# Performance work log

Hardware: AMD Instinct MI355X
Metric: run time of the kernel (lower is better)

Reference implementation:

```python
import jax, jax.numpy as jnp
import numpy as np

NEG_INF = float("-inf")
WINDOW = 5  # window_size in LocalAttention; half = WINDOW // 2 = 2


def setup_inputs() -> dict:
    key = jax.random.key(0)
    kq, kk, kv = jax.random.split(key, 3)
    B, L, H, E = 4, 2048, 8, 64
    queries = jax.random.normal(kq, (B, L, H, E), dtype=jnp.float32)
    keys = jax.random.normal(kk, (B, L, H, E), dtype=jnp.float32)
    values = jax.random.normal(kv, (B, L, H, E), dtype=jnp.float32)
    return {"queries": queries, "keys": keys, "values": values}


def reference(queries, keys, values):
    # queries/keys/values: [B, L, H, E]; dropout is identity (eval mode).
    B, L, H, E = queries.shape
    scale = 1.0 / jnp.sqrt(jnp.asarray(E, dtype=queries.dtype))
    # Shared scores for both branches: [B, H, L, S]
    scores = jnp.einsum("blhe,bshe->bhls", queries, keys)

    # Global (unmasked) branch
    A_global = jax.nn.softmax(scale * scores, axis=-1)

    # Local branch: torch mask allows j in [max(i-2,0), min(i+2,L)) => i-2 <= j <= i+1
    half = WINDOW // 2
    i = jnp.arange(L)[:, None]
    j = jnp.arange(L)[None, :]
    allowed = (j - i >= -half) & (j - i < half)  # [L, L], asymmetric window
    local_scores = jnp.where(allowed, scores, NEG_INF)
    A_local = jax.nn.softmax(scale * local_scores, axis=-1)

    # Sum of the two attention outputs == (A_global + A_local) @ V
    out = jnp.einsum("bhls,bshd->blhd", A_global + A_local, values)
    return out
```

## Files before the change

### kernel.cpp

```cpp
#include <hip/hip_runtime.h>
#include <hip/hip_bf16.h>
#include <stdint.h>


#define LQ 2048
#define HQ 8
#define EQ 64
#define BQ 4
#define BM 64
#define BN 64
#define RS (HQ * EQ)
#define SCALE_LOG2E 0.18033688011112042f
#define NTILE (LQ / BN)
#define TILE_U32 2048
#define IMG_U32 (BQ * HQ * NTILE * TILE_U32)

typedef __attribute__((ext_vector_type(8))) short bf16x8;
typedef __attribute__((ext_vector_type(4))) float f32x4;
typedef __attribute__((ext_vector_type(4))) unsigned int u32x4;

static __device__ __forceinline__ unsigned int f2bf(float f) {
    union { float f; unsigned int u; } c; c.f = f;
    return (c.u + 0x8000u) >> 16;
}
static __device__ __forceinline__ unsigned int pk2(float lo, float hi) {
    union { float f; unsigned int u; } a, b; a.f = lo; b.f = hi;
    return ((a.u + 0x8000u) >> 16) | ((b.u + 0x8000u) & 0xffff0000u);
}
static __device__ __forceinline__ void gload16(const uint32_t* g, void* l) {
    __builtin_amdgcn_global_load_lds(
        (const __attribute__((address_space(1))) unsigned int*)g,
        (__attribute__((address_space(3))) unsigned int*)l, 16, 0, 0);
}

__global__ __launch_bounds__(256) void prepack_kernel(
    const float* __restrict__ K, const float* __restrict__ V,
    uint32_t* __restrict__ Kimg, uint32_t* __restrict__ Vimg)
{
    const int tid = threadIdx.x;
    const int jc  = blockIdx.x;
    const int bh  = blockIdx.y;
    const int b   = bh >> 3;
    const int h   = bh & 7;
    const int j0  = jc * BN;
    const float* Kbh = K + (size_t)b * LQ * RS + h * EQ;
    const float* Vbh = V + (size_t)b * LQ * RS + h * EQ;
    uint32_t* Kt = Kimg + (size_t)(bh * NTILE + jc) * TILE_U32;
    uint32_t* Vt = Vimg + (size_t)(bh * NTILE + jc) * TILE_U32;

    #pragma unroll
    for (int it = 0; it < 2; ++it) {
        int t2 = tid + it * 256;
        int jr = t2 >> 3, eo = t2 & 7;
        const float* src = Kbh + (size_t)(j0 + jr) * RS + eo * 8;
        float4 a  = *(const float4*)src;
        float4 bv = *(const float4*)(src + 4);
        u32x4 p;
        p.x = pk2(a.x, a.y);   p.y = pk2(a.z, a.w);
        p.z = pk2(bv.x, bv.y); p.w = pk2(bv.z, bv.w);
        *(u32x4*)&Kt[jr * 32 + ((eo ^ (jr & 7)) << 2)] = p;
    }
    #pragma unroll
    for (int it = 0; it < 2; ++it) {
        int t2 = tid + it * 256;
        int e = t2 & 63, jo = t2 >> 6;
        const float* src = Vbh + (size_t)(j0 + jo * 8) * RS + e;
        float v0 = src[0 * RS], v1 = src[1 * RS], v2 = src[2 * RS], v3 = src[3 * RS];
        float v4 = src[4 * RS], v5 = src[5 * RS], v6 = src[6 * RS], v7 = src[7 * RS];
        u32x4 p;
        p.x = pk2(v0, v1); p.y = pk2(v2, v3);
        p.z = pk2(v4, v5); p.w = pk2(v6, v7);
        *(u32x4*)&Vt[e * 32 + ((jo ^ (e & 7)) << 2)] = p;
    }
}

__global__ __launch_bounds__(256) void hybrid_attn_fast(
    const float* __restrict__ Q, const float* __restrict__ K,
    const float* __restrict__ V, const uint32_t* __restrict__ Kimg,
    const uint32_t* __restrict__ Vimg, float* __restrict__ O)
{
    __shared__ unsigned short Ks[64 * 64];
    __shared__ unsigned short Vt[64 * 64];
    __shared__ unsigned short Ps[4][16 * 64];
    __shared__ float sloc[BM][4];

    const int tid  = threadIdx.x;
    const int wave = tid >> 6;
    const int lane = tid & 63;
    const int c    = lane & 15;
    const int g    = lane >> 4;
    const int qt   = blockIdx.x;
    const int bh   = blockIdx.y;
    const int b    = bh >> 3;
    const int h    = bh & 7;
    const int i0   = qt * BM;

    const float* Qbh = Q + (size_t)b * LQ * RS + h * EQ;
    const float* Kbh = K + (size_t)b * LQ * RS + h * EQ;
    const float* Vbh = V + (size_t)b * LQ * RS + h * EQ;
    float*       Obh = O + (size_t)b * LQ * RS + h * EQ;

    bf16x8 qf[2];
    {
        const int iA = i0 + wave * 16 + c;
        const float* qrow = Qbh + (size_t)iA * RS + g * 8;
        #pragma unroll
        for (int f = 0; f < 2; ++f) {
            float4 a  = *(const float4*)(qrow + f * 32);
            float4 bv = *(const float4*)(qrow + f * 32 + 4);
            union { bf16x8 v; unsigned int u[4]; } fr;
            fr.u[0] = pk2(a.x  * SCALE_LOG2E, a.y  * SCALE_LOG2E);
            fr.u[1] = pk2(a.z  * SCALE_LOG2E, a.w  * SCALE_LOG2E);
            fr.u[2] = pk2(bv.x * SCALE_LOG2E, bv.y * SCALE_LOG2E);
            fr.u[3] = pk2(bv.z * SCALE_LOG2E, bv.w * SCALE_LOG2E);
            qf[f] = fr.v;
        }
    }

    int kfo[4][2], vfo[4][2], pfo[2], pso[4][4];
    #pragma unroll
    for (int n = 0; n < 4; ++n)
        #pragma unroll
        for (int f = 0; f < 2; ++f)
            kfo[n][f] = (n * 16 + c) * 64 + ((((f << 2) | g) ^ (c & 7)) << 3);
    #pragma unroll
    for (int eg = 0; eg < 4; ++eg)
        #pragma unroll
        for (int kh = 0; kh < 2; ++kh)
            vfo[eg][kh] = (eg * 16 + c) * 64 + ((((kh << 2) | g) ^ (c & 7)) << 3);
    #pragma unroll
    for (int kh = 0; kh < 2; ++kh)
        pfo[kh] = c * 64 + ((((kh << 2) | g) ^ (c & 7)) << 3);
    #pragma unroll
    for (int r = 0; r < 4; ++r) {
        const int row = g * 4 + r;
        #pragma unroll
        for (int n = 0; n < 4; ++n) {
            const int col = n * 16 + c;
            pso[r][n] = row * 64 + ((((col >> 3) ^ (row & 7)) << 3) | (col & 7));
        }
    }

    f32x4 oacc[4];
    #pragma unroll
    for (int eg = 0; eg < 4; ++eg) oacc[eg] = (f32x4){0.f, 0.f, 0.f, 0.f};
    float l_r[4] = {0.f, 0.f, 0.f, 0.f};

    const uint32_t* kgb = Kimg + (size_t)bh * (NTILE * TILE_U32) + (wave * 2) * 256 + lane * 4;
    const uint32_t* vgb = Vimg + (size_t)bh * (NTILE * TILE_U32) + (wave * 2) * 256 + lane * 4;
    unsigned short* ksl0 = &Ks[(wave * 2) * 512];
    unsigned short* ksl1 = &Ks[(wave * 2 + 1) * 512];
    unsigned short* vtl0 = &Vt[(wave * 2) * 512];
    unsigned short* vtl1 = &Vt[(wave * 2 + 1) * 512];

    for (int jc = 0; jc < NTILE; ++jc) {
        __syncthreads();
        const uint32_t* kg = kgb + jc * TILE_U32;
        const uint32_t* vg = vgb + jc * TILE_U32;
        gload16(kg,       ksl0);
        gload16(kg + 256, ksl1);
        gload16(vg,       vtl0);
        gload16(vg + 256, vtl1);
        __syncthreads();

        f32x4 sf[4];
        #pragma unroll
        for (int n = 0; n < 4; ++n) {
            bf16x8 k0 = *(const bf16x8*)&Ks[kfo[n][0]];
            bf16x8 k1 = *(const bf16x8*)&Ks[kfo[n][1]];
            f32x4 acc = (f32x4){0.f, 0.f, 0.f, 0.f};
            acc = __builtin_amdgcn_mfma_f32_16x16x32_bf16(qf[0], k0, acc, 0, 0, 0);
            acc = __builtin_amdgcn_mfma_f32_16x16x32_bf16(qf[1], k1, acc, 0, 0, 0);
            sf[n] = acc;
        }

        #pragma unroll
        for (int r = 0; r < 4; ++r) {
            float p0 = exp2f(sf[0][r]);
            float p1 = exp2f(sf[1][r]);
            float p2 = exp2f(sf[2][r]);
            float p3 = exp2f(sf[3][r]);
            l_r[r] += (p0 + p1) + (p2 + p3);
            Ps[wave][pso[r][0]] = (unsigned short)f2bf(p0);
            Ps[wave][pso[r][1]] = (unsigned short)f2bf(p1);
            Ps[wave][pso[r][2]] = (unsigned short)f2bf(p2);
            Ps[wave][pso[r][3]] = (unsigned short)f2bf(p3);
        }
        asm volatile("s_waitcnt lgkmcnt(0)" ::: "memory");

        bf16x8 pf0 = *(const bf16x8*)&Ps[wave][pfo[0]];
        bf16x8 pf1 = *(const bf16x8*)&Ps[wave][pfo[1]];
        #pragma unroll
        for (int eg = 0; eg < 4; ++eg) {
            bf16x8 v0 = *(const bf16x8*)&Vt[vfo[eg][0]];
            bf16x8 v1 = *(const bf16x8*)&Vt[vfo[eg][1]];
            oacc[eg] = __builtin_amdgcn_mfma_f32_16x16x32_bf16(pf0, v0, oacc[eg], 0, 0, 0);
            oacc[eg] = __builtin_amdgcn_mfma_f32_16x16x32_bf16(pf1, v1, oacc[eg], 0, 0, 0);
        }
    }

    #pragma unroll
    for (int r = 0; r < 4; ++r) {
        float l = l_r[r];
        l += __shfl_xor(l, 1);
        l += __shfl_xor(l, 2);
        l += __shfl_xor(l, 4);
        l += __shfl_xor(l, 8);
        l_r[r] = 1.0f / l;
    }

    {
        const int br = tid >> 2;
        const int jj = tid & 3;
        const int i  = i0 + br;
        const int j  = i - 2 + jj;
        float s = -INFINITY;
        if (j >= 0 && j < LQ) {
            const float* qrow = Qbh + (size_t)i * RS;
            const float* krow = Kbh + (size_t)j * RS;
            float acc = 0.f;
            #pragma unroll
            for (int e = 0; e < 64; e += 4) {
                float4 qa = *(const float4*)(qrow + e);
                float4 ka = *(const float4*)(krow + e);
                acc = fmaf(qa.x, ka.x, acc); acc = fmaf(qa.y, ka.y, acc);
                acc = fmaf(qa.z, ka.z, acc); acc = fmaf(qa.w, ka.w, acc);
            }
            s = 0.125f * acc;
        }
        sloc[br][jj] = s;
    }
    __syncthreads();

    #pragma unroll
    for (int r = 0; r < 4; ++r) {
        const int row = wave * 16 + g * 4 + r;
        const int i   = i0 + row;
        float s0 = sloc[row][0], s1 = sloc[row][1], s2 = sloc[row][2], s3 = sloc[row][3];
        float mx = fmaxf(fmaxf(s0, s1), fmaxf(s2, s3));
        float w0 = expf(s0 - mx), w1 = expf(s1 - mx);
        float w2 = expf(s2 - mx), w3 = expf(s3 - mx);
        float inv = 1.0f / (w0 + w1 + w2 + w3);
        w0 *= inv; w1 *= inv; w2 *= inv; w3 *= inv;
        const float li = l_r[r];
        float* orow = Obh + (size_t)i * RS;
        #pragma unroll
        for (int eg = 0; eg < 4; ++eg) {
            const int e = eg * 16 + c;
            float val = oacc[eg][r] * li;
            if (w0 > 0.f) val += w0 * Vbh[(size_t)(i - 2) * RS + e];
            if (w1 > 0.f) val += w1 * Vbh[(size_t)(i - 1) * RS + e];
            if (w2 > 0.f) val += w2 * Vbh[(size_t)(i    ) * RS + e];
            if (w3 > 0.f) val += w3 * Vbh[(size_t)(i + 1) * RS + e];
            orow[e] = val;
        }
    }
}

__global__ __launch_bounds__(256) void hybrid_attn_fb(
    const float* __restrict__ Q, const float* __restrict__ K,
    const float* __restrict__ V, float* __restrict__ O)
{
    __shared__ unsigned short Ks[64 * 64];
    __shared__ unsigned short Vt[64 * 64];
    __shared__ unsigned short Ps[4][16 * 64];
    __shared__ float sloc[BM][4];

    const int tid  = threadIdx.x;
    const int wave = tid >> 6;
    const int lane = tid & 63;
    const int c    = lane & 15;
    const int g    = lane >> 4;
    const int qt   = blockIdx.x;
    const int bh   = blockIdx.y;
    const int b    = bh >> 3;
    const int h    = bh & 7;
    const int i0   = qt * BM;

    const float* Qbh = Q + (size_t)b * LQ * RS + h * EQ;
    const float* Kbh = K + (size_t)b * LQ * RS + h * EQ;
    const float* Vbh = V + (size_t)b * LQ * RS + h * EQ;
    float*       Obh = O + (size_t)b * LQ * RS + h * EQ;

    bf16x8 qf[2];
    {
        const int iA = i0 + wave * 16 + c;
        const float* qrow = Qbh + (size_t)iA * RS + g * 8;
        #pragma unroll
        for (int f = 0; f < 2; ++f) {
            float4 a  = *(const float4*)(qrow + f * 32);
            float4 bv = *(const float4*)(qrow + f * 32 + 4);
            union { bf16x8 v; unsigned int u[4]; } fr;
            fr.u[0] = pk2(a.x  * SCALE_LOG2E, a.y  * SCALE_LOG2E);
            fr.u[1] = pk2(a.z  * SCALE_LOG2E, a.w  * SCALE_LOG2E);
            fr.u[2] = pk2(bv.x * SCALE_LOG2E, bv.y * SCALE_LOG2E);
            fr.u[3] = pk2(bv.z * SCALE_LOG2E, bv.w * SCALE_LOG2E);
            qf[f] = fr.v;
        }
    }

    int kfo[4][2], vfo[4][2], pfo[2], pso[4][4];
    #pragma unroll
    for (int n = 0; n < 4; ++n)
        #pragma unroll
        for (int f = 0; f < 2; ++f)
            kfo[n][f] = (n * 16 + c) * 64 + ((((f << 2) | g) ^ (c & 7)) << 3);
    #pragma unroll
    for (int eg = 0; eg < 4; ++eg)
        #pragma unroll
        for (int kh = 0; kh < 2; ++kh)
            vfo[eg][kh] = (eg * 16 + c) * 64 + ((((kh << 2) | g) ^ (c & 7)) << 3);
    #pragma unroll
    for (int kh = 0; kh < 2; ++kh)
        pfo[kh] = c * 64 + ((((kh << 2) | g) ^ (c & 7)) << 3);
    #pragma unroll
    for (int r = 0; r < 4; ++r) {
        const int row = g * 4 + r;
        #pragma unroll
        for (int n = 0; n < 4; ++n) {
            const int col = n * 16 + c;
            pso[r][n] = row * 64 + ((((col >> 3) ^ (row & 7)) << 3) | (col & 7));
        }
    }

    f32x4 oacc[4];
    #pragma unroll
    for (int eg = 0; eg < 4; ++eg) oacc[eg] = (f32x4){0.f, 0.f, 0.f, 0.f};
    float l_r[4] = {0.f, 0.f, 0.f, 0.f};

    for (int j0 = 0; j0 < LQ; j0 += BN) {
        __syncthreads();
        #pragma unroll
        for (int it = 0; it < 2; ++it) {
            int t2 = tid + it * 256;
            int jr = t2 >> 3, eo = t2 & 7;
            const float* src = Kbh + (size_t)(j0 + jr) * RS + eo * 8;
            float4 a  = *(const float4*)src;
            float4 bv = *(const float4*)(src + 4);
            u32x4 p;
            p.x = pk2(a.x, a.y);   p.y = pk2(a.z, a.w);
            p.z = pk2(bv.x, bv.y); p.w = pk2(bv.z, bv.w);
            *(u32x4*)&Ks[jr * 64 + ((eo ^ (jr & 7)) << 3)] = p;
        }
        #pragma unroll
        for (int it = 0; it < 2; ++it) {
            int t2 = tid + it * 256;
            int e = t2 & 63, jo = t2 >> 6;
            const float* src = Vbh + (size_t)(j0 + jo * 8) * RS + e;
            float v0 = src[0 * RS], v1 = src[1 * RS], v2 = src[2 * RS], v3 = src[3 * RS];
            float v4 = src[4 * RS], v5 = src[5 * RS], v6 = src[6 * RS], v7 = src[7 * RS];
            u32x4 p;
            p.x = pk2(v0, v1); p.y = pk2(v2, v3);
            p.z = pk2(v4, v5); p.w = pk2(v6, v7);
            *(u32x4*)&Vt[e * 64 + ((jo ^ (e & 7)) << 3)] = p;
        }
        __syncthreads();

        f32x4 sf[4];
        #pragma unroll
        for (int n = 0; n < 4; ++n) {
            bf16x8 k0 = *(const bf16x8*)&Ks[kfo[n][0]];
            bf16x8 k1 = *(const bf16x8*)&Ks[kfo[n][1]];
            f32x4 acc = (f32x4){0.f, 0.f, 0.f, 0.f};
            acc = __builtin_amdgcn_mfma_f32_16x16x32_bf16(qf[0], k0, acc, 0, 0, 0);
            acc = __builtin_amdgcn_mfma_f32_16x16x32_bf16(qf[1], k1, acc, 0, 0, 0);
            sf[n] = acc;
        }
        #pragma unroll
        for (int r = 0; r < 4; ++r) {
            float p0 = exp2f(sf[0][r]);
            float p1 = exp2f(sf[1][r]);
            float p2 = exp2f(sf[2][r]);
            float p3 = exp2f(sf[3][r]);
            l_r[r] += (p0 + p1) + (p2 + p3);
            Ps[wave][pso[r][0]] = (unsigned short)f2bf(p0);
            Ps[wave][pso[r][1]] = (unsigned short)f2bf(p1);
            Ps[wave][pso[r][2]] = (unsigned short)f2bf(p2);
            Ps[wave][pso[r][3]] = (unsigned short)f2bf(p3);
        }
        asm volatile("s_waitcnt lgkmcnt(0)" ::: "memory");

        bf16x8 pf0 = *(const bf16x8*)&Ps[wave][pfo[0]];
        bf16x8 pf1 = *(const bf16x8*)&Ps[wave][pfo[1]];
        #pragma unroll
        for (int eg = 0; eg < 4; ++eg) {
            bf16x8 v0 = *(const bf16x8*)&Vt[vfo[eg][0]];
            bf16x8 v1 = *(const bf16x8*)&Vt[vfo[eg][1]];
            oacc[eg] = __builtin_amdgcn_mfma_f32_16x16x32_bf16(pf0, v0, oacc[eg], 0, 0, 0);
            oacc[eg] = __builtin_amdgcn_mfma_f32_16x16x32_bf16(pf1, v1, oacc[eg], 0, 0, 0);
        }
    }

    #pragma unroll
    for (int r = 0; r < 4; ++r) {
        float l = l_r[r];
        l += __shfl_xor(l, 1);
        l += __shfl_xor(l, 2);
        l += __shfl_xor(l, 4);
        l += __shfl_xor(l, 8);
        l_r[r] = 1.0f / l;
    }

    {
        const int br = tid >> 2;
        const int jj = tid & 3;
        const int i  = i0 + br;
        const int j  = i - 2 + jj;
        float s = -INFINITY;
        if (j >= 0 && j < LQ) {
            const float* qrow = Qbh + (size_t)i * RS;
            const float* krow = Kbh + (size_t)j * RS;
            float acc = 0.f;
            #pragma unroll
            for (int e = 0; e < 64; e += 4) {
                float4 qa = *(const float4*)(qrow + e);
                float4 ka = *(const float4*)(krow + e);
                acc = fmaf(qa.x, ka.x, acc); acc = fmaf(qa.y, ka.y, acc);
                acc = fmaf(qa.z, ka.z, acc); acc = fmaf(qa.w, ka.w, acc);
            }
            s = 0.125f * acc;
        }
        sloc[br][jj] = s;
    }
    __syncthreads();

    #pragma unroll
    for (int r = 0; r < 4; ++r) {
        const int row = wave * 16 + g * 4 + r;
        const int i   = i0 + row;
        float s0 = sloc[row][0], s1 = sloc[row][1], s2 = sloc[row][2], s3 = sloc[row][3];
        float mx = fmaxf(fmaxf(s0, s1), fmaxf(s2, s3));
        float w0 = expf(s0 - mx), w1 = expf(s1 - mx);
        float w2 = expf(s2 - mx), w3 = expf(s3 - mx);
        float inv = 1.0f / (w0 + w1 + w2 + w3);
        w0 *= inv; w1 *= inv; w2 *= inv; w3 *= inv;
        const float li = l_r[r];
        float* orow = Obh + (size_t)i * RS;
        #pragma unroll
        for (int eg = 0; eg < 4; ++eg) {
            const int e = eg * 16 + c;
            float val = oacc[eg][r] * li;
            if (w0 > 0.f) val += w0 * Vbh[(size_t)(i - 2) * RS + e];
            if (w1 > 0.f) val += w1 * Vbh[(size_t)(i - 1) * RS + e];
            if (w2 > 0.f) val += w2 * Vbh[(size_t)(i    ) * RS + e];
            if (w3 > 0.f) val += w3 * Vbh[(size_t)(i + 1) * RS + e];
            orow[e] = val;
        }
    }
}

extern "C" void kernel_launch(void* const* d_in, const int* in_sizes, int n_in,
                              void* d_out, int out_size, void* d_ws, size_t ws_size,
                              hipStream_t stream) {
    (void)in_sizes; (void)n_in; (void)out_size;
    const float* Q = (const float*)d_in[0];
    const float* K = (const float*)d_in[1];
    const float* V = (const float*)d_in[2];
    float* O = (float*)d_out;
    dim3 grid(LQ / BM, BQ * HQ);
    const size_t need = (size_t)2 * IMG_U32 * 4;
    if (ws_size >= need) {
        uint32_t* Kimg = (uint32_t*)d_ws;
        uint32_t* Vimg = Kimg + IMG_U32;
        hipLaunchKernelGGL(prepack_kernel, dim3(NTILE, BQ * HQ), dim3(256), 0, stream,
                           K, V, Kimg, Vimg);
        hipLaunchKernelGGL(hybrid_attn_fast, grid, dim3(256), 0, stream,
                           Q, K, V, Kimg, Vimg, O);
    } else {
        hipLaunchKernelGGL(hybrid_attn_fb, grid, dim3(256), 0, stream, Q, K, V, O);
    }
}
```

Baseline: 179.8 us.

## Restructure fast attention kernel to two-wave blocks with 32 rows per wave

```diff
diff --git a/kernel.cpp b/kernel.cpp
--- a/kernel.cpp
+++ b/kernel.cpp
@@ -18,14 +18,16 @@
 typedef __attribute__((ext_vector_type(8))) short bf16x8;
 typedef __attribute__((ext_vector_type(4))) float f32x4;
 typedef __attribute__((ext_vector_type(4))) unsigned int u32x4;
-
-static __device__ __forceinline__ unsigned int f2bf(float f) {
-    union { float f; unsigned int u; } c; c.f = f;
-    return (c.u + 0x8000u) >> 16;
-}
+typedef __attribute__((ext_vector_type(2))) unsigned int u32x2;
+
 static __device__ __forceinline__ unsigned int pk2(float lo, float hi) {
     union { float f; unsigned int u; } a, b; a.f = lo; b.f = hi;
     return ((a.u + 0x8000u) >> 16) | ((b.u + 0x8000u) & 0xffff0000u);
+}
+static __device__ __forceinline__ float fexp2(float x) {
+    float r;
+    asm volatile("v_exp_f32 %0, %1\n\ts_nop 1" : "=v"(r) : "v"(x));
+    return r;
 }
 static __device__ __forceinline__ void gload16(const uint32_t* g, void* l) {
     __builtin_amdgcn_global_load_lds(
@@ -74,14 +76,13 @@
     }
 }
 
-__global__ __launch_bounds__(256) void hybrid_attn_fast(
+__global__ __launch_bounds__(128, 2) void hybrid_attn_v3(
     const float* __restrict__ Q, const float* __restrict__ K,
     const float* __restrict__ V, const uint32_t* __restrict__ Kimg,
     const uint32_t* __restrict__ Vimg, float* __restrict__ O)
 {
-    __shared__ unsigned short Ks[64 * 64];
-    __shared__ unsigned short Vt[64 * 64];
-    __shared__ unsigned short Ps[4][16 * 64];
+    __shared__ unsigned short KV[8192];
+    __shared__ unsigned short Pt[2][2048];
     __shared__ float sloc[BM][4];
 
     const int tid  = threadIdx.x;
@@ -94,6 +95,214 @@
     const int b    = bh >> 3;
     const int h    = bh & 7;
     const int i0   = qt * BM;
+    const int c7   = c & 7;
+    const int sw   = (c & 3) << 1;
+
+    const float* Qbh = Q + (size_t)b * LQ * RS + h * EQ;
+    const float* Kbh = K + (size_t)b * LQ * RS + h * EQ;
+    const float* Vbh = V + (size_t)b * LQ * RS + h * EQ;
+    float*       Obh = O + (size_t)b * LQ * RS + h * EQ;
+
+    bf16x8 qf[2][2];
+    #pragma unroll
+    for (int t = 0; t < 2; ++t) {
+        const int iq = i0 + wave * 32 + t * 16 + c;
+        const float* qrow = Qbh + (size_t)iq * RS + g * 8;
+        #pragma unroll
+        for (int f = 0; f < 2; ++f) {
+            float4 a  = *(const float4*)(qrow + f * 32);
+            float4 bv = *(const float4*)(qrow + f * 32 + 4);
+            union { bf16x8 v; unsigned int u[4]; } fr;
+            fr.u[0] = pk2(a.x  * SCALE_LOG2E, a.y  * SCALE_LOG2E);
+            fr.u[1] = pk2(a.z  * SCALE_LOG2E, a.w  * SCALE_LOG2E);
+            fr.u[2] = pk2(bv.x * SCALE_LOG2E, bv.y * SCALE_LOG2E);
+            fr.u[3] = pk2(bv.z * SCALE_LOG2E, bv.w * SCALE_LOG2E);
+            qf[t][f] = fr.v;
+        }
+    }
+
+    unsigned short* kvb0 = &KV[c * 64 + (((0 << 2) | g) ^ c7) * 8];
+    unsigned short* kvb1 = &KV[c * 64 + (((1 << 2) | g) ^ c7) * 8];
+    unsigned short* pw0 = &Pt[wave][c * 64 + (((0 * 4 + g) ^ sw) << 2)];
+    unsigned short* pw1 = &Pt[wave][c * 64 + (((1 * 4 + g) ^ sw) << 2)];
+    unsigned short* pw2 = &Pt[wave][c * 64 + (((2 * 4 + g) ^ sw) << 2)];
+    unsigned short* pw3 = &Pt[wave][c * 64 + (((3 * 4 + g) ^ sw) << 2)];
+    unsigned short* pr = &Pt[wave][c * 64 + (((g << 1) ^ sw) << 2)];
+
+    const uint32_t* kg0 = Kimg + (size_t)bh * (NTILE * TILE_U32) + tid * 4;
+    const uint32_t* vg0 = Vimg + (size_t)bh * (NTILE * TILE_U32) + tid * 4;
+
+    f32x4 oacc[2][4];
+    #pragma unroll
+    for (int t = 0; t < 2; ++t)
+        #pragma unroll
+        for (int eg = 0; eg < 4; ++eg) oacc[t][eg] = (f32x4){0.f, 0.f, 0.f, 0.f};
+    float lsum[2] = {0.f, 0.f};
+
+    for (int jc = 0; jc < NTILE; ++jc) {
+        __syncthreads();
+        const uint32_t* kg = kg0 + jc * TILE_U32;
+        const uint32_t* vg = vg0 + jc * TILE_U32;
+        #pragma unroll
+        for (int kk = 0; kk < 4; ++kk)
+            gload16(kg + kk * 512, &KV[kk * 1024 + wave * 512]);
+        #pragma unroll
+        for (int kk = 0; kk < 4; ++kk)
+            gload16(vg + kk * 512, &KV[4096 + kk * 1024 + wave * 512]);
+        __syncthreads();
+
+        bf16x8 kfr[4][2];
+        #pragma unroll
+        for (int n = 0; n < 4; ++n) {
+            kfr[n][0] = *(const bf16x8*)&kvb0[n * 1024];
+            kfr[n][1] = *(const bf16x8*)&kvb1[n * 1024];
+        }
+
+        #pragma unroll
+        for (int t = 0; t < 2; ++t) {
+            f32x4 sf[4];
+            #pragma unroll
+            for (int n = 0; n < 4; ++n) {
+                f32x4 acc = (f32x4){0.f, 0.f, 0.f, 0.f};
+                acc = __builtin_amdgcn_mfma_f32_16x16x32_bf16(kfr[n][0], qf[t][0], acc, 0, 0, 0);
+                acc = __builtin_amdgcn_mfma_f32_16x16x32_bf16(kfr[n][1], qf[t][1], acc, 0, 0, 0);
+                sf[n] = acc;
+            }
+            float ls = 0.f;
+            #pragma unroll
+            for (int n = 0; n < 4; ++n) {
+                float p0 = fexp2(sf[n][0]);
+                float p1 = fexp2(sf[n][1]);
+                float p2 = fexp2(sf[n][2]);
+                float p3 = fexp2(sf[n][3]);
+                ls += (p0 + p1) + (p2 + p3);
+                u32x2 pkd;
+                pkd.x = pk2(p0, p1);
+                pkd.y = pk2(p2, p3);
+                unsigned short* dst = (n == 0 ? pw0 : n == 1 ? pw1 : n == 2 ? pw2 : pw3);
+                *(u32x2*)(dst + t * 1024) = pkd;
+            }
+            lsum[t] += ls;
+        }
+        asm volatile("s_waitcnt lgkmcnt(0)" ::: "memory");
+
+        bf16x8 pfr[2][2];
+        #pragma unroll
+        for (int t = 0; t < 2; ++t) {
+            pfr[t][0] = *(const bf16x8*)&pr[t * 1024];
+            pfr[t][1] = *(const bf16x8*)&pr[t * 1024 + 32];
+        }
+        #pragma unroll
+        for (int eg = 0; eg < 4; ++eg) {
+            bf16x8 v0 = *(const bf16x8*)&kvb0[4096 + eg * 1024];
+            bf16x8 v1 = *(const bf16x8*)&kvb1[4096 + eg * 1024];
+            #pragma unroll
+            for (int t = 0; t < 2; ++t) {
+                oacc[t][eg] = __builtin_amdgcn_mfma_f32_16x16x32_bf16(v0, pfr[t][0], oacc[t][eg], 0, 0, 0);
+                oacc[t][eg] = __builtin_amdgcn_mfma_f32_16x16x32_bf16(v1, pfr[t][1], oacc[t][eg], 0, 0, 0);
+            }
+        }
+    }
+
+    float linv[2];
+    #pragma unroll
+    for (int t = 0; t < 2; ++t) {
+        float l = lsum[t];
+        l += __shfl_xor(l, 16);
+        l += __shfl_xor(l, 32);
+        linv[t] = 1.0f / l;
+    }
+
+    {
+        const int br = tid >> 1;
+        const int i  = i0 + br;
+        const float* qrow = Qbh + (size_t)i * RS;
+        #pragma unroll
+        for (int half = 0; half < 2; ++half) {
+            const int jj = (tid & 1) * 2 + half;
+            const int j  = i - 2 + jj;
+            float s = -INFINITY;
+            if (j >= 0 && j < LQ) {
+                const float* krow = Kbh + (size_t)j * RS;
+                float acc = 0.f;
+                #pragma unroll
+                for (int e = 0; e < 64; e += 4) {
+                    float4 qa = *(const float4*)(qrow + e);
+                    float4 ka = *(const float4*)(krow + e);
+                    acc = fmaf(qa.x, ka.x, acc); acc = fmaf(qa.y, ka.y, acc);
+                    acc = fmaf(qa.z, ka.z, acc); acc = fmaf(qa.w, ka.w, acc);
+                }
+                s = 0.125f * acc;
+            }
+            sloc[br][jj] = s;
+        }
+    }
+    __syncthreads();
+
+    #pragma unroll
+    for (int t = 0; t < 2; ++t) {
+        const int row = wave * 32 + t * 16 + c;
+        const int i   = i0 + row;
+        float s0 = sloc[row][0], s1 = sloc[row][1], s2 = sloc[row][2], s3 = sloc[row][3];
+        float mx = fmaxf(fmaxf(s0, s1), fmaxf(s2, s3));
+        float w0 = expf(s0 - mx), w1 = expf(s1 - mx);
+        float w2 = expf(s2 - mx), w3 = expf(s3 - mx);
+        float inv = 1.0f / (w0 + w1 + w2 + w3);
+        w0 *= inv; w1 *= inv; w2 *= inv; w3 *= inv;
+        const float li = linv[t];
+        float* orow = Obh + (size_t)i * RS;
+        #pragma unroll
+        for (int eg = 0; eg < 4; ++eg) {
+            const int e0 = eg * 16 + g * 4;
+            float v0 = oacc[t][eg][0] * li;
+            float v1 = oacc[t][eg][1] * li;
+            float v2 = oacc[t][eg][2] * li;
+            float v3 = oacc[t][eg][3] * li;
+            if (w0 > 0.f) {
+                float4 vv = *(const float4*)(Vbh + (size_t)(i - 2) * RS + e0);
+                v0 = fmaf(w0, vv.x, v0); v1 = fmaf(w0, vv.y, v1);
+                v2 = fmaf(w0, vv.z, v2); v3 = fmaf(w0, vv.w, v3);
+            }
+            if (w1 > 0.f) {
+                float4 vv = *(const float4*)(Vbh + (size_t)(i - 1) * RS + e0);
+                v0 = fmaf(w1, vv.x, v0); v1 = fmaf(w1, vv.y, v1);
+                v2 = fmaf(w1, vv.z, v2); v3 = fmaf(w1, vv.w, v3);
+            }
+            {
+                float4 vv = *(const float4*)(Vbh + (size_t)i * RS + e0);
+                v0 = fmaf(w2, vv.x, v0); v1 = fmaf(w2, vv.y, v1);
+                v2 = fmaf(w2, vv.z, v2); v3 = fmaf(w2, vv.w, v3);
+            }
+            if (w3 > 0.f) {
+                float4 vv = *(const float4*)(Vbh + (size_t)(i + 1) * RS + e0);
+                v0 = fmaf(w3, vv.x, v0); v1 = fmaf(w3, vv.y, v1);
+                v2 = fmaf(w3, vv.z, v2); v3 = fmaf(w3, vv.w, v3);
+            }
+            float4 outv; outv.x = v0; outv.y = v1; outv.z = v2; outv.w = v3;
+            *(float4*)(orow + e0) = outv;
+        }
+    }
+}
+
+__global__ __launch_bounds__(256) void hybrid_attn_fb(
+    const float* __restrict__ Q, const float* __restrict__ K,
+    const float* __restrict__ V, float* __restrict__ O)
+{
+    __shared__ unsigned short Ks[64 * 64];
+    __shared__ unsigned short Vt[64 * 64];
+    __shared__ unsigned short Ps[4][16 * 64];
+    __shared__ float sloc[BM][4];
+
+    const int tid  = threadIdx.x;
+    const int wave = tid >> 6;
+    const int lane = tid & 63;
+    const int c    = lane & 15;
+    const int g    = lane >> 4;
+    const int qt   = blockIdx.x;
+    const int bh   = blockIdx.y;
+    const int b    = bh >> 3;
+    const int h    = bh & 7;
+    const int i0   = qt * BM;
 
     const float* Qbh = Q + (size_t)b * LQ * RS + h * EQ;
     const float* Kbh = K + (size_t)b * LQ * RS + h * EQ;
@@ -146,21 +355,32 @@
     for (int eg = 0; eg < 4; ++eg) oacc[eg] = (f32x4){0.f, 0.f, 0.f, 0.f};
     float l_r[4] = {0.f, 0.f, 0.f, 0.f};
 
-    const uint32_t* kgb = Kimg + (size_t)bh * (NTILE * TILE_U32) + (wave * 2) * 256 + lane * 4;
-    const uint32_t* vgb = Vimg + (size_t)bh * (NTILE * TILE_U32) + (wave * 2) * 256 + lane * 4;
-    unsigned short* ksl0 = &Ks[(wave * 2) * 512];
-    unsigned short* ksl1 = &Ks[(wave * 2 + 1) * 512];
-    unsigned short* vtl0 = &Vt[(wave * 2) * 512];
-    unsigned short* vtl1 = &Vt[(wave * 2 + 1) * 512];
-
-    for (int jc = 0; jc < NTILE; ++jc) {
+    for (int j0 = 0; j0 < LQ; j0 += BN) {
         __syncthreads();
-        const uint32_t* kg = kgb + jc * TILE_U32;
-        const uint32_t* vg = vgb + jc * TILE_U32;
-        gload16(kg,       ksl0);
-        gload16(kg + 256, ksl1);
-        gload16(vg,       vtl0);
-        gload16(vg + 256, vtl1);
+        #pragma unroll
+        for (int it = 0; it < 2; ++it) {
+            int t2 = tid + it * 256;
+            int jr = t2 >> 3, eo = t2 & 7;
+            const float* src = Kbh + (size_t)(j0 + jr) * RS + eo * 8;
+            float4 a  = *(const float4*)src;
+            float4 bv = *(const float4*)(src + 4);
+            u32x4 p;
+            p.x = pk2(a.x, a.y);   p.y = pk2(a.z, a.w);
+            p.z = pk2(bv.x, bv.y); p.w = pk2(bv.z, bv.w);
+            *(u32x4*)&Ks[jr * 64 + ((eo ^ (jr & 7)) << 3)] = p;
+        }
+        #pragma unroll
+        for (int it = 0; it < 2; ++it) {
+            int t2 = tid + it * 256;
+            int e = t2 & 63, jo = t2 >> 6;
+            const float* src = Vbh + (size_t)(j0 + jo * 8) * RS + e;
+            float v0 = src[0 * RS], v1 = src[1 * RS], v2 = src[2 * RS], v3 = src[3 * RS];
+            float v4 = src[4 * RS], v5 = src[5 * RS], v6 = src[6 * RS], v7 = src[7 * RS];
+            u32x4 p;
+            p.x = pk2(v0, v1); p.y = pk2(v2, v3);
+            p.z = pk2(v4, v5); p.w = pk2(v6, v7);
+            *(u32x4*)&Vt[e * 64 + ((jo ^ (e & 7)) << 3)] = p;
+        }
         __syncthreads();
 
         f32x4 sf[4];
@@ -173,18 +393,17 @@
             acc = __builtin_amdgcn_mfma_f32_16x16x32_bf16(qf[1], k1, acc, 0, 0, 0);
             sf[n] = acc;
         }
-
         #pragma unroll
         for (int r = 0; r < 4; ++r) {
-            float p0 = exp2f(sf[0][r]);
-            float p1 = exp2f(sf[1][r]);
-            float p2 = exp2f(sf[2][r]);
-            float p3 = exp2f(sf[3][r]);
+            float p0 = fexp2(sf[0][r]);
+            float p1 = fexp2(sf[1][r]);
+            float p2 = fexp2(sf[2][r]);
+            float p3 = fexp2(sf[3][r]);
             l_r[r] += (p0 + p1) + (p2 + p3);
-            Ps[wave][pso[r][0]] = (unsigned short)f2bf(p0);
-            Ps[wave][pso[r][1]] = (unsigned short)f2bf(p1);
-            Ps[wave][pso[r][2]] = (unsigned short)f2bf(p2);
-            Ps[wave][pso[r][3]] = (unsigned short)f2bf(p3);
+            Ps[wave][pso[r][0]] = (unsigned short)(pk2(p0, 0.f) & 0xffff);
+            Ps[wave][pso[r][1]] = (unsigned short)(pk2(p1, 0.f) & 0xffff);
+            Ps[wave][pso[r][2]] = (unsigned short)(pk2(p2, 0.f) & 0xffff);
+            Ps[wave][pso[r][3]] = (unsigned short)(pk2(p3, 0.f) & 0xffff);
         }
         asm volatile("s_waitcnt lgkmcnt(0)" ::: "memory");
 
@@ -257,198 +476,6 @@
     }
 }
 
-__global__ __launch_bounds__(256) void hybrid_attn_fb(
-    const float* __restrict__ Q, const float* __restrict__ K,
-    const float* __restrict__ V, float* __restrict__ O)
-{
-    __shared__ unsigned short Ks[64 * 64];
-    __shared__ unsigned short Vt[64 * 64];
-    __shared__ unsigned short Ps[4][16 * 64];
-    __shared__ float sloc[BM][4];
-
-    const int tid  = threadIdx.x;
-    const int wave = tid >> 6;
-    const int lane = tid & 63;
-    const int c    = lane & 15;
-    const int g    = lane >> 4;
-    const int qt   = blockIdx.x;
-    const int bh   = blockIdx.y;
-    const int b    = bh >> 3;
-    const int h    = bh & 7;
-    const int i0   = qt * BM;
-
-    const float* Qbh = Q + (size_t)b * LQ * RS + h * EQ;
-    const float* Kbh = K + (size_t)b * LQ * RS + h * EQ;
-    const float* Vbh = V + (size_t)b * LQ * RS + h * EQ;
-    float*       Obh = O + (size_t)b * LQ * RS + h * EQ;
-
-    bf16x8 qf[2];
-    {
-        const int iA = i0 + wave * 16 + c;
-        const float* qrow = Qbh + (size_t)iA * RS + g * 8;
-        #pragma unroll
-        for (int f = 0; f < 2; ++f) {
-            float4 a  = *(const float4*)(qrow + f * 32);
-            float4 bv = *(const float4*)(qrow + f * 32 + 4);
-            union { bf16x8 v; unsigned int u[4]; } fr;
-            fr.u[0] = pk2(a.x  * SCALE_LOG2E, a.y  * SCALE_LOG2E);
-            fr.u[1] = pk2(a.z  * SCALE_LOG2E, a.w  * SCALE_LOG2E);
-            fr.u[2] = pk2(bv.x * SCALE_LOG2E, bv.y * SCALE_LOG2E);
-            fr.u[3] = pk2(bv.z * SCALE_LOG2E, bv.w * SCALE_LOG2E);
-            qf[f] = fr.v;
-        }
-    }
-
-    int kfo[4][2], vfo[4][2], pfo[2], pso[4][4];
-    #pragma unroll
-    for (int n = 0; n < 4; ++n)
-        #pragma unroll
-        for (int f = 0; f < 2; ++f)
-            kfo[n][f] = (n * 16 + c) * 64 + ((((f << 2) | g) ^ (c & 7)) << 3);
-    #pragma unroll
-    for (int eg = 0; eg < 4; ++eg)
-        #pragma unroll
-        for (int kh = 0; kh < 2; ++kh)
-            vfo[eg][kh] = (eg * 16 + c) * 64 + ((((kh << 2) | g) ^ (c & 7)) << 3);
-    #pragma unroll
-    for (int kh = 0; kh < 2; ++kh)
-        pfo[kh] = c * 64 + ((((kh << 2) | g) ^ (c & 7)) << 3);
-    #pragma unroll
-    for (int r = 0; r < 4; ++r) {
-        const int row = g * 4 + r;
-        #pragma unroll
-        for (int n = 0; n < 4; ++n) {
-            const int col = n * 16 + c;
-            pso[r][n] = row * 64 + ((((col >> 3) ^ (row & 7)) << 3) | (col & 7));
-        }
-    }
-
-    f32x4 oacc[4];
-    #pragma unroll
-    for (int eg = 0; eg < 4; ++eg) oacc[eg] = (f32x4){0.f, 0.f, 0.f, 0.f};
-    float l_r[4] = {0.f, 0.f, 0.f, 0.f};
-
-    for (int j0 = 0; j0 < LQ; j0 += BN) {
-        __syncthreads();
-        #pragma unroll
-        for (int it = 0; it < 2; ++it) {
-            int t2 = tid + it * 256;
-            int jr = t2 >> 3, eo = t2 & 7;
-            const float* src = Kbh + (size_t)(j0 + jr) * RS + eo * 8;
-            float4 a  = *(const float4*)src;
-            float4 bv = *(const float4*)(src + 4);
-            u32x4 p;
-            p.x = pk2(a.x, a.y);   p.y = pk2(a.z, a.w);
-            p.z = pk2(bv.x, bv.y); p.w = pk2(bv.z, bv.w);
-            *(u32x4*)&Ks[jr * 64 + ((eo ^ (jr & 7)) << 3)] = p;
-        }
-        #pragma unroll
-        for (int it = 0; it < 2; ++it) {
-            int t2 = tid + it * 256;
-            int e = t2 & 63, jo = t2 >> 6;
-            const float* src = Vbh + (size_t)(j0 + jo * 8) * RS + e;
-            float v0 = src[0 * RS], v1 = src[1 * RS], v2 = src[2 * RS], v3 = src[3 * RS];
-            float v4 = src[4 * RS], v5 = src[5 * RS], v6 = src[6 * RS], v7 = src[7 * RS];
-            u32x4 p;
-            p.x = pk2(v0, v1); p.y = pk2(v2, v3);
-            p.z = pk2(v4, v5); p.w = pk2(v6, v7);
-            *(u32x4*)&Vt[e * 64 + ((jo ^ (e & 7)) << 3)] = p;
-        }
-        __syncthreads();
-
-        f32x4 sf[4];
-        #pragma unroll
-        for (int n = 0; n < 4; ++n) {
-            bf16x8 k0 = *(const bf16x8*)&Ks[kfo[n][0]];
-            bf16x8 k1 = *(const bf16x8*)&Ks[kfo[n][1]];
-            f32x4 acc = (f32x4){0.f, 0.f, 0.f, 0.f};
-            acc = __builtin_amdgcn_mfma_f32_16x16x32_bf16(qf[0], k0, acc, 0, 0, 0);
-            acc = __builtin_amdgcn_mfma_f32_16x16x32_bf16(qf[1], k1, acc, 0, 0, 0);
-            sf[n] = acc;
-        }
-        #pragma unroll
-        for (int r = 0; r < 4; ++r) {
-            float p0 = exp2f(sf[0][r]);
-            float p1 = exp2f(sf[1][r]);
-            float p2 = exp2f(sf[2][r]);
-            float p3 = exp2f(sf[3][r]);
-            l_r[r] += (p0 + p1) + (p2 + p3);
-            Ps[wave][pso[r][0]] = (unsigned short)f2bf(p0);
-            Ps[wave][pso[r][1]] = (unsigned short)f2bf(p1);
-            Ps[wave][pso[r][2]] = (unsigned short)f2bf(p2);
-            Ps[wave][pso[r][3]] = (unsigned short)f2bf(p3);
-        }
-        asm volatile("s_waitcnt lgkmcnt(0)" ::: "memory");
-
-        bf16x8 pf0 = *(const bf16x8*)&Ps[wave][pfo[0]];
-        bf16x8 pf1 = *(const bf16x8*)&Ps[wave][pfo[1]];
-        #pragma unroll
-        for (int eg = 0; eg < 4; ++eg) {
-            bf16x8 v0 = *(const bf16x8*)&Vt[vfo[eg][0]];
-            bf16x8 v1 = *(const bf16x8*)&Vt[vfo[eg][1]];
-            oacc[eg] = __builtin_amdgcn_mfma_f32_16x16x32_bf16(pf0, v0, oacc[eg], 0, 0, 0);
-            oacc[eg] = __builtin_amdgcn_mfma_f32_16x16x32_bf16(pf1, v1, oacc[eg], 0, 0, 0);
-        }
-    }
-
-    #pragma unroll
-    for (int r = 0; r < 4; ++r) {
-        float l = l_r[r];
-        l += __shfl_xor(l, 1);
-        l += __shfl_xor(l, 2);
-        l += __shfl_xor(l, 4);
-        l += __shfl_xor(l, 8);
-        l_r[r] = 1.0f / l;
-    }
-
-    {
-        const int br = tid >> 2;
-        const int jj = tid & 3;
-        const int i  = i0 + br;
-        const int j  = i - 2 + jj;
-        float s = -INFINITY;
-        if (j >= 0 && j < LQ) {
-            const float* qrow = Qbh + (size_t)i * RS;
-            const float* krow = Kbh + (size_t)j * RS;
-            float acc = 0.f;
-            #pragma unroll
-            for (int e = 0; e < 64; e += 4) {
-                float4 qa = *(const float4*)(qrow + e);
-                float4 ka = *(const float4*)(krow + e);
-                acc = fmaf(qa.x, ka.x, acc); acc = fmaf(qa.y, ka.y, acc);
-                acc = fmaf(qa.z, ka.z, acc); acc = fmaf(qa.w, ka.w, acc);
-            }
-            s = 0.125f * acc;
-        }
-        sloc[br][jj] = s;
-    }
-    __syncthreads();
-
-    #pragma unroll
-    for (int r = 0; r < 4; ++r) {
-        const int row = wave * 16 + g * 4 + r;
-        const int i   = i0 + row;
-        float s0 = sloc[row][0], s1 = sloc[row][1], s2 = sloc[row][2], s3 = sloc[row][3];
-        float mx = fmaxf(fmaxf(s0, s1), fmaxf(s2, s3));
-        float w0 = expf(s0 - mx), w1 = expf(s1 - mx);
-        float w2 = expf(s2 - mx), w3 = expf(s3 - mx);
-        float inv = 1.0f / (w0 + w1 + w2 + w3);
-        w0 *= inv; w1 *= inv; w2 *= inv; w3 *= inv;
-        const float li = l_r[r];
-        float* orow = Obh + (size_t)i * RS;
-        #pragma unroll
-        for (int eg = 0; eg < 4; ++eg) {
-            const int e = eg * 16 + c;
-            float val = oacc[eg][r] * li;
-            if (w0 > 0.f) val += w0 * Vbh[(size_t)(i - 2) * RS + e];
-            if (w1 > 0.f) val += w1 * Vbh[(size_t)(i - 1) * RS + e];
-            if (w2 > 0.f) val += w2 * Vbh[(size_t)(i    ) * RS + e];
-            if (w3 > 0.f) val += w3 * Vbh[(size_t)(i + 1) * RS + e];
-            orow[e] = val;
-        }
-    }
-}
-
 extern "C" void kernel_launch(void* const* d_in, const int* in_sizes, int n_in,
                               void* d_out, int out_size, void* d_ws, size_t ws_size,
                               hipStream_t stream) {
@@ -457,16 +484,16 @@
     const float* K = (const float*)d_in[1];
     const float* V = (const float*)d_in[2];
     float* O = (float*)d_out;
-    dim3 grid(LQ / BM, BQ * HQ);
     const size_t need = (size_t)2 * IMG_U32 * 4;
     if (ws_size >= need) {
         uint32_t* Kimg = (uint32_t*)d_ws;
         uint32_t* Vimg = Kimg + IMG_U32;
         hipLaunchKernelGGL(prepack_kernel, dim3(NTILE, BQ * HQ), dim3(256), 0, stream,
                            K, V, Kimg, Vimg);
-        hipLaunchKernelGGL(hybrid_attn_fast, grid, dim3(256), 0, stream,
+        hipLaunchKernelGGL(hybrid_attn_v3, dim3(LQ / BM, BQ * HQ), dim3(128), 0, stream,
                            Q, K, V, Kimg, Vimg, O);
     } else {
-        hipLaunchKernelGGL(hybrid_attn_fb, grid, dim3(256), 0, stream, Q, K, V, O);
-    }
-}
+        hipLaunchKernelGGL(hybrid_attn_fb, dim3(LQ / BM, BQ * HQ), dim3(256), 0, stream,
+                           Q, K, V, O);
+    }
+}
```

Result: faster. 166.0 us (-7.6%).
